# Performance work log

Measured on AMD Instinct MI355X. Metric: run time of the kernel, lower is better.

Reference implementation:

```python
import jax, jax.numpy as jnp
import numpy as np
from jax import lax

LBDA = 0.1
EPS = 0.01
NUM_CLASSES = 20


def setup_inputs() -> dict:
    key = jax.random.key(0)
    k1, k2 = jax.random.split(key)
    target_features = jax.random.normal(k1, (2048, 8, 2048), dtype=jnp.float32)
    support_features = jax.random.normal(k2, (100, 8, 2048), dtype=jnp.float32)
    # 20-way 5-shot: every class present so per-class mean is well defined
    support_labels = jnp.repeat(jnp.arange(NUM_CLASSES, dtype=jnp.int32), 100 // NUM_CLASSES)
    return {
        "target_features": target_features,
        "support_features": support_features,
        "support_labels": support_labels,
    }


def _softmin(xs, lbda):
    # -lbda * log(sum_i exp(-x_i/lbda)), stable
    return -lbda * jax.nn.logsumexp(jnp.stack([-x / lbda for x in xs], axis=0), axis=0)


def otam_cum_dist(dists, lbda=LBDA):
    # dists: [Q, Sp, L, S] frame distance matrices
    d = jnp.pad(dists, ((0, 0), (0, 0), (0, 0), (1, 1)))  # pad columns -> M = S + 2
    M = d.shape[-1]
    # row 0: running sum along columns (cum[0,0] = d[0,0] = 0 from padding)
    row0 = jnp.cumsum(d[:, :, 0, :], axis=-1)

    def step(prev_row, d_row):
        # prev_row, d_row: [Q, Sp, M]; column 0 is never written -> stays 0
        cur = [jnp.zeros_like(d_row[..., 0])]
        cur.append(d_row[..., 1] + _softmin([prev_row[..., 0], prev_row[..., 1], cur[0]], lbda))
        for m in range(2, M - 1):
            cur.append(d_row[..., m] + _softmin([prev_row[..., m - 1], cur[m - 1]], lbda))
        cur.append(d_row[..., M - 1] + _softmin([prev_row[..., M - 2], prev_row[..., M - 1], cur[M - 2]], lbda))
        new_row = jnp.stack(cur, axis=-1)
        return new_row, None

    d_rows = jnp.moveaxis(d[:, :, 1:, :], 2, 0)  # [L-1, Q, Sp, M]
    final_row, _ = lax.scan(step, row0, d_rows)
    return final_row[..., -1]  # [Q, Sp]


def cos_sim(x, y, eps=EPS):
    num = x @ y.T
    den = jnp.linalg.norm(x, axis=-1)[:, None] * jnp.linalg.norm(y, axis=-1)[None, :] + eps
    return num / den


def reference(target_features, support_features, support_labels):
    Q, S, D = target_features.shape
    Sp = support_features.shape[0]
    tf = target_features.reshape(Q * S, D)
    sf = support_features.reshape(Sp * S, D)
    frame_dists = 1.0 - cos_sim(tf, sf)  # [Q*S, Sp*S]
    # '(tb ts) (sb ss) -> tb sb ts ss'
    dists = frame_dists.reshape(Q, S, Sp, S).transpose(0, 2, 1, 3)
    cum_dists = otam_cum_dist(dists) + otam_cum_dist(dists.transpose(0, 1, 3, 2))  # [Q, Sp]
    # per-class mean over support (torch.unique returns sorted labels 0..C-1)
    onehot = (support_labels[:, None] == jnp.arange(NUM_CLASSES)[None, :]).astype(cum_dists.dtype)
    onehot = onehot / jnp.sum(onehot, axis=0, keepdims=True)
    class_dists = cum_dists @ onehot  # [Q, C]
    return -class_dists[None]  # logits [1, Q, C]
```

## Files before the change

### kernel.cpp

```cpp
#include <hip/hip_runtime.h>

#define QN    2048
#define SS    8
#define DD    2048
#define SP    100
#define NCLS  20
#define MROWS (QN*SS)
#define NROWS (SP*SS)
#define NPAD  896
#define KK    DD

typedef __bf16 bf16x8 __attribute__((ext_vector_type(8)));
typedef float  f32x4  __attribute__((ext_vector_type(4)));

__device__ __forceinline__ unsigned short f2bf(float f) {
    unsigned int u = __float_as_uint(f);
    u += 0x7fffu + ((u >> 16) & 1u);
    return (unsigned short)(u >> 16);
}

__global__ void cvt_kernel(const float* __restrict__ tf, const float* __restrict__ sf,
                           unsigned short* __restrict__ Abf, unsigned short* __restrict__ Bbf,
                           float* __restrict__ nA, float* __restrict__ nB)
{
    int row = blockIdx.x;
    int tid = threadIdx.x;
    const float* src = nullptr;
    unsigned short* dst;
    float* nrm; int r;
    if (row < MROWS) { src = tf + (size_t)row * DD; dst = Abf + (size_t)row * DD; nrm = nA; r = row; }
    else {
        r = row - MROWS;
        dst = Bbf + (size_t)r * DD; nrm = nB;
        if (r < NROWS) src = sf + (size_t)r * DD;
    }
    float s = 0.f;
    union { uint4 u; unsigned short h[8]; } pk;
    if (src) {
        float4 v0 = *(const float4*)(src + tid * 8);
        float4 v1 = *(const float4*)(src + tid * 8 + 4);
        s = v0.x*v0.x + v0.y*v0.y + v0.z*v0.z + v0.w*v0.w
          + v1.x*v1.x + v1.y*v1.y + v1.z*v1.z + v1.w*v1.w;
        pk.h[0]=f2bf(v0.x); pk.h[1]=f2bf(v0.y); pk.h[2]=f2bf(v0.z); pk.h[3]=f2bf(v0.w);
        pk.h[4]=f2bf(v1.x); pk.h[5]=f2bf(v1.y); pk.h[6]=f2bf(v1.z); pk.h[7]=f2bf(v1.w);
    } else {
        pk.u = make_uint4(0, 0, 0, 0);
    }
    *(uint4*)(dst + (size_t)tid * 8) = pk.u;

    for (int o = 32; o; o >>= 1) s += __shfl_down(s, o);
    __shared__ float red[4];
    if ((tid & 63) == 0) red[tid >> 6] = s;
    __syncthreads();
    if (tid == 0) nrm[r] = sqrtf(red[0] + red[1] + red[2] + red[3]);
}

__device__ __forceinline__ void gld16(const void* g, void* l) {
    __builtin_amdgcn_global_load_lds(
        (const __attribute__((address_space(1))) unsigned int*)g,
        (__attribute__((address_space(3))) unsigned int*)l, 16, 0, 0);
}

__global__ __launch_bounds__(256, 2) void gemm_kernel(
    const unsigned short* __restrict__ A,
    const unsigned short* __restrict__ B,
    const float* __restrict__ nA, const float* __restrict__ nB,
    float* __restrict__ Dout)
{
    __shared__ __align__(16) unsigned short Als[128 * 32];
    __shared__ __align__(16) unsigned short Bls[128 * 32];
    const int mt  = blockIdx.x;
    const int nt  = blockIdx.y;
    const int tid = threadIdx.x;
    const int lane = tid & 63;
    const int w    = tid >> 6;
    const int wm   = (w & 1) * 64, wn = (w >> 1) * 64;
    const int col  = lane & 15, kg = lane >> 4;

    f32x4 acc[4][4] = {};

    const int c0 = tid, c1 = tid + 256;
    const unsigned short* Ab0 = A + (size_t)mt * 128 * KK + (size_t)(c0 >> 2) * KK + (c0 & 3) * 8;
    const unsigned short* Ab1 = A + (size_t)mt * 128 * KK + (size_t)(c1 >> 2) * KK + (c1 & 3) * 8;
    const unsigned short* Bb0 = B + (size_t)nt * 128 * KK + (size_t)(c0 >> 2) * KK + (c0 & 3) * 8;
    const unsigned short* Bb1 = B + (size_t)nt * 128 * KK + (size_t)(c1 >> 2) * KK + (c1 & 3) * 8;

    for (int kk = 0; kk < KK; kk += 32) {
        __syncthreads();
        gld16(Ab0 + kk, (char*)Als + c0 * 16);
        gld16(Ab1 + kk, (char*)Als + c1 * 16);
        gld16(Bb0 + kk, (char*)Bls + c0 * 16);
        gld16(Bb1 + kk, (char*)Bls + c1 * 16);
        __syncthreads();
        bf16x8 af[4], bfr[4];
#pragma unroll
        for (int i = 0; i < 4; i++) af[i]  = *(const bf16x8*)(Als + (wm + i * 16 + col) * 32 + kg * 8);
#pragma unroll
        for (int i = 0; i < 4; i++) bfr[i] = *(const bf16x8*)(Bls + (wn + i * 16 + col) * 32 + kg * 8);
#pragma unroll
        for (int mi = 0; mi < 4; mi++)
#pragma unroll
            for (int ni = 0; ni < 4; ni++)
                acc[mi][ni] = __builtin_amdgcn_mfma_f32_16x16x32_bf16(af[mi], bfr[ni], acc[mi][ni], 0, 0, 0);
    }

    const int mbase = mt * 128 + wm;
    const int nbase = nt * 128 + wn;
#pragma unroll
    for (int ni = 0; ni < 4; ni++) {
        int n = nbase + ni * 16 + col;
        if (n < NROWS) {
            float ny = nB[n];
#pragma unroll
            for (int mi = 0; mi < 4; mi++) {
#pragma unroll
                for (int r = 0; r < 4; r++) {
                    int m = mbase + mi * 16 + kg * 4 + r;
                    float nx = nA[m];
                    Dout[(size_t)m * NROWS + n] = 1.0f - acc[mi][ni][r] / (nx * ny + 0.01f);
                }
            }
        }
    }
}

__device__ __forceinline__ float softmin2(float a, float b) {
    float mn = fminf(a, b), mx = fmaxf(a, b);
    return mn - 0.1f * __logf(1.0f + __expf((mn - mx) * 10.0f));
}
__device__ __forceinline__ float softmin3(float a, float b, float c) {
    float mn = fminf(fminf(a, b), c);
    float sum = __expf((mn - a) * 10.0f) + __expf((mn - b) * 10.0f) + __expf((mn - c) * 10.0f);
    return mn - 0.1f * __logf(sum);
}

__global__ void dp_kernel(const float* __restrict__ dist, float* __restrict__ cum)
{
    int idx = blockIdx.x * 256 + threadIdx.x;
    int q = idx / SP, sp = idx % SP;
    float t[8][8];
    const float* base = dist + (size_t)q * 8 * NROWS + sp * 8;
#pragma unroll
    for (int i = 0; i < 8; i++) {
        float4 a = *(const float4*)(base + (size_t)i * NROWS);
        float4 b = *(const float4*)(base + (size_t)i * NROWS + 4);
        t[i][0]=a.x; t[i][1]=a.y; t[i][2]=a.z; t[i][3]=a.w;
        t[i][4]=b.x; t[i][5]=b.y; t[i][6]=b.z; t[i][7]=b.w;
    }
    float res = 0.f;
#pragma unroll
    for (int dir = 0; dir < 2; dir++) {
        float prev[10], cur[10];
        prev[0] = 0.f;
#pragma unroll
        for (int m = 1; m <= 8; m++) prev[m] = prev[m - 1] + (dir ? t[m - 1][0] : t[0][m - 1]);
        prev[9] = prev[8];
#pragma unroll
        for (int l = 1; l < 8; l++) {
            cur[0] = 0.f;
            cur[1] = (dir ? t[0][l] : t[l][0]) + softmin3(prev[0], prev[1], 0.0f);
#pragma unroll
            for (int m = 2; m <= 8; m++)
                cur[m] = (dir ? t[m - 1][l] : t[l][m - 1]) + softmin2(prev[m - 1], cur[m - 1]);
            cur[9] = softmin3(prev[8], prev[9], cur[8]);
#pragma unroll
            for (int m = 0; m < 10; m++) prev[m] = cur[m];
        }
        res += prev[9];
    }
    cum[idx] = res;
}

__global__ void cls_kernel(const float* __restrict__ cum, const int* __restrict__ labels,
                           float* __restrict__ out)
{
    int idx = blockIdx.x * 256 + threadIdx.x;
    int q = idx / NCLS, c = idx % NCLS;
    float s = 0.f; int n = 0;
    const float* row = cum + (size_t)q * SP;
    for (int sp = 0; sp < SP; sp++) {
        if (labels[sp] == c) { s += row[sp]; n++; }
    }
    out[idx] = -s / (float)n;
}

extern "C" void kernel_launch(void* const* d_in, const int* in_sizes, int n_in,
                              void* d_out, int out_size, void* d_ws, size_t ws_size,
                              hipStream_t stream)
{
    const float* tf     = (const float*)d_in[0];
    const float* sf     = (const float*)d_in[1];
    const int*   labels = (const int*)d_in[2];
    float* out = (float*)d_out;

    char* ws = (char*)d_ws;
    const size_t szA    = (size_t)MROWS * KK * 2;
    const size_t szB    = (size_t)NPAD  * KK * 2;
    const size_t szNA   = (size_t)MROWS * 4;
    const size_t szNB   = (size_t)NPAD  * 4;
    const size_t szDist = (size_t)MROWS * NROWS * 4;
    unsigned short* Abf = (unsigned short*)ws;
    unsigned short* Bbf = (unsigned short*)(ws + szA);
    float* nA   = (float*)(ws + szA + szB);
    float* nB   = (float*)(ws + szA + szB + szNA);
    float* dist = (float*)(ws + szA + szB + szNA + szNB);
    float* cum  = (float*)(ws + szA + szB + szNA + szNB + szDist);

    cvt_kernel<<<MROWS + NPAD, 256, 0, stream>>>(tf, sf, Abf, Bbf, nA, nB);
    gemm_kernel<<<dim3(128, 7), 256, 0, stream>>>(Abf, Bbf, nA, nB, dist);
    dp_kernel<<<800, 256, 0, stream>>>(dist, cum);
    cls_kernel<<<160, 256, 0, stream>>>(cum, labels, out);
}
```

Before: 319.0 us.

## Fuse OTAM DP into GEMM epilogue via LDS and swizzle LDS tiles

The GEMM epilogue now writes normalized cosine distances into an LDS staging buffer. The OTAM dynamic programme runs directly from there, with lanes split by direction and the two directions combined by a shuffle. This drops the separate dp kernel and the round trip of the full fp32 distance matrix through global memory. A XOR swizzle on the k-offset of the A/B LDS tiles is also added to reduce bank conflicts. LDS per block grows to about 33KB, which may affect occupancy at two blocks per CU, and the DP now runs inside the GEMM blocks.

```diff
diff --git a/kernel.cpp b/kernel.cpp
--- a/kernel.cpp
+++ b/kernel.cpp
@@ -55,20 +55,34 @@
     if (tid == 0) nrm[r] = sqrtf(red[0] + red[1] + red[2] + red[3]);
 }
 
+__device__ __forceinline__ float softmin2(float a, float b) {
+    float mn = fminf(a, b), mx = fmaxf(a, b);
+    return mn - 0.1f * __logf(1.0f + __expf((mn - mx) * 10.0f));
+}
+__device__ __forceinline__ float softmin3(float a, float b, float c) {
+    float mn = fminf(fminf(a, b), c);
+    float sum = __expf((mn - a) * 10.0f) + __expf((mn - b) * 10.0f) + __expf((mn - c) * 10.0f);
+    return mn - 0.1f * __logf(sum);
+}
+
 __device__ __forceinline__ void gld16(const void* g, void* l) {
     __builtin_amdgcn_global_load_lds(
         (const __attribute__((address_space(1))) unsigned int*)g,
         (__attribute__((address_space(3))) unsigned int*)l, 16, 0, 0);
 }
 
+#define EPB (32 * 65)
+
 __global__ __launch_bounds__(256, 2) void gemm_kernel(
     const unsigned short* __restrict__ A,
     const unsigned short* __restrict__ B,
     const float* __restrict__ nA, const float* __restrict__ nB,
-    float* __restrict__ Dout)
-{
-    __shared__ __align__(16) unsigned short Als[128 * 32];
-    __shared__ __align__(16) unsigned short Bls[128 * 32];
+    float* __restrict__ cum)
+{
+    __shared__ __align__(16) char smem[4 * EPB * 4];
+    unsigned short* Als = (unsigned short*)smem;
+    unsigned short* Bls = Als + 128 * 32;
+
     const int mt  = blockIdx.x;
     const int nt  = blockIdx.y;
     const int tid = threadIdx.x;
@@ -80,10 +94,14 @@
     f32x4 acc[4][4] = {};
 
     const int c0 = tid, c1 = tid + 256;
-    const unsigned short* Ab0 = A + (size_t)mt * 128 * KK + (size_t)(c0 >> 2) * KK + (c0 & 3) * 8;
-    const unsigned short* Ab1 = A + (size_t)mt * 128 * KK + (size_t)(c1 >> 2) * KK + (c1 & 3) * 8;
-    const unsigned short* Bb0 = B + (size_t)nt * 128 * KK + (size_t)(c0 >> 2) * KK + (c0 & 3) * 8;
-    const unsigned short* Bb1 = B + (size_t)nt * 128 * KK + (size_t)(c1 >> 2) * KK + (c1 & 3) * 8;
+    const int r0 = c0 >> 2, k0 = ((c0 & 3) ^ ((c0 >> 3) & 3)) * 8;
+    const int r1 = c1 >> 2, k1 = ((c1 & 3) ^ ((c1 >> 3) & 3)) * 8;
+    const unsigned short* Ab0 = A + (size_t)mt * 128 * KK + (size_t)r0 * KK + k0;
+    const unsigned short* Ab1 = A + (size_t)mt * 128 * KK + (size_t)r1 * KK + k1;
+    const unsigned short* Bb0 = B + (size_t)nt * 128 * KK + (size_t)r0 * KK + k0;
+    const unsigned short* Bb1 = B + (size_t)nt * 128 * KK + (size_t)r1 * KK + k1;
+
+    const int ksw = (kg ^ ((col >> 1) & 3)) * 8;
 
     for (int kk = 0; kk < KK; kk += 32) {
         __syncthreads();
@@ -94,9 +112,9 @@
         __syncthreads();
         bf16x8 af[4], bfr[4];
 #pragma unroll
-        for (int i = 0; i < 4; i++) af[i]  = *(const bf16x8*)(Als + (wm + i * 16 + col) * 32 + kg * 8);
-#pragma unroll
-        for (int i = 0; i < 4; i++) bfr[i] = *(const bf16x8*)(Bls + (wn + i * 16 + col) * 32 + kg * 8);
+        for (int i = 0; i < 4; i++) af[i]  = *(const bf16x8*)(Als + (wm + i * 16 + col) * 32 + ksw);
+#pragma unroll
+        for (int i = 0; i < 4; i++) bfr[i] = *(const bf16x8*)(Bls + (wn + i * 16 + col) * 32 + ksw);
 #pragma unroll
         for (int mi = 0; mi < 4; mi++)
 #pragma unroll
@@ -106,69 +124,65 @@
 
     const int mbase = mt * 128 + wm;
     const int nbase = nt * 128 + wn;
-#pragma unroll
-    for (int ni = 0; ni < 4; ni++) {
-        int n = nbase + ni * 16 + col;
-        if (n < NROWS) {
-            float ny = nB[n];
-#pragma unroll
-            for (int mi = 0; mi < 4; mi++) {
-#pragma unroll
-                for (int r = 0; r < 4; r++) {
-                    int m = mbase + mi * 16 + kg * 4 + r;
-                    float nx = nA[m];
-                    Dout[(size_t)m * NROWS + n] = 1.0f - acc[mi][ni][r] / (nx * ny + 0.01f);
-                }
+    const int qv0 = mt * 16 + (wm >> 3);
+    const int sv0 = nt * 16 + (wn >> 3);
+    float* eb = (float*)smem + w * EPB;
+
+    const int qv2 = (lane >> 3) & 3;
+    const int sv  = lane & 7;
+    const int dir = lane >> 5;
+
+#pragma unroll
+    for (int p = 0; p < 2; p++) {
+        __syncthreads();
+#pragma unroll
+        for (int mi2 = 0; mi2 < 2; mi2++) {
+            const int mi = p * 2 + mi2;
+            const float nx0 = nA[mbase + mi * 16 + kg * 4 + 0];
+            const float nx1 = nA[mbase + mi * 16 + kg * 4 + 1];
+            const float nx2 = nA[mbase + mi * 16 + kg * 4 + 2];
+            const float nx3 = nA[mbase + mi * 16 + kg * 4 + 3];
+#pragma unroll
+            for (int ni = 0; ni < 4; ni++) {
+                const float ny = nB[nbase + ni * 16 + col];
+                float* dstp = eb + (mi2 * 16 + kg * 4) * 65 + ni * 16 + col;
+                dstp[0]      = 1.0f - acc[mi][ni][0] / (nx0 * ny + 0.01f);
+                dstp[65]     = 1.0f - acc[mi][ni][1] / (nx1 * ny + 0.01f);
+                dstp[130]    = 1.0f - acc[mi][ni][2] / (nx2 * ny + 0.01f);
+                dstp[195]    = 1.0f - acc[mi][ni][3] / (nx3 * ny + 0.01f);
             }
         }
-    }
-}
-
-__device__ __forceinline__ float softmin2(float a, float b) {
-    float mn = fminf(a, b), mx = fmaxf(a, b);
-    return mn - 0.1f * __logf(1.0f + __expf((mn - mx) * 10.0f));
-}
-__device__ __forceinline__ float softmin3(float a, float b, float c) {
-    float mn = fminf(fminf(a, b), c);
-    float sum = __expf((mn - a) * 10.0f) + __expf((mn - b) * 10.0f) + __expf((mn - c) * 10.0f);
-    return mn - 0.1f * __logf(sum);
-}
-
-__global__ void dp_kernel(const float* __restrict__ dist, float* __restrict__ cum)
-{
-    int idx = blockIdx.x * 256 + threadIdx.x;
-    int q = idx / SP, sp = idx % SP;
-    float t[8][8];
-    const float* base = dist + (size_t)q * 8 * NROWS + sp * 8;
-#pragma unroll
-    for (int i = 0; i < 8; i++) {
-        float4 a = *(const float4*)(base + (size_t)i * NROWS);
-        float4 b = *(const float4*)(base + (size_t)i * NROWS + 4);
-        t[i][0]=a.x; t[i][1]=a.y; t[i][2]=a.z; t[i][3]=a.w;
-        t[i][4]=b.x; t[i][5]=b.y; t[i][6]=b.z; t[i][7]=b.w;
-    }
-    float res = 0.f;
-#pragma unroll
-    for (int dir = 0; dir < 2; dir++) {
+        __syncthreads();
+
+        const float* tb = eb + (qv2 * 8) * 65 + sv * 8;
         float prev[10], cur[10];
         prev[0] = 0.f;
 #pragma unroll
-        for (int m = 1; m <= 8; m++) prev[m] = prev[m - 1] + (dir ? t[m - 1][0] : t[0][m - 1]);
+        for (int m = 1; m <= 8; m++)
+            prev[m] = prev[m - 1] + (dir ? tb[(m - 1) * 65] : tb[m - 1]);
         prev[9] = prev[8];
 #pragma unroll
         for (int l = 1; l < 8; l++) {
+            float d[8];
+#pragma unroll
+            for (int j = 0; j < 8; j++) d[j] = dir ? tb[j * 65 + l] : tb[l * 65 + j];
             cur[0] = 0.f;
-            cur[1] = (dir ? t[0][l] : t[l][0]) + softmin3(prev[0], prev[1], 0.0f);
+            cur[1] = d[0] + softmin3(prev[0], prev[1], 0.0f);
 #pragma unroll
             for (int m = 2; m <= 8; m++)
-                cur[m] = (dir ? t[m - 1][l] : t[l][m - 1]) + softmin2(prev[m - 1], cur[m - 1]);
+                cur[m] = d[m - 1] + softmin2(prev[m - 1], cur[m - 1]);
             cur[9] = softmin3(prev[8], prev[9], cur[8]);
 #pragma unroll
             for (int m = 0; m < 10; m++) prev[m] = cur[m];
         }
-        res += prev[9];
-    }
-    cum[idx] = res;
+        float res = prev[9];
+        res += __shfl_down(res, 32);
+        if (dir == 0) {
+            const int qg = qv0 + p * 4 + qv2;
+            const int sg = sv0 + sv;
+            if (sg < SP) cum[(size_t)qg * SP + sg] = res;
+        }
+    }
 }
 
 __global__ void cls_kernel(const float* __restrict__ cum, const int* __restrict__ labels,
@@ -198,16 +212,13 @@
     const size_t szB    = (size_t)NPAD  * KK * 2;
     const size_t szNA   = (size_t)MROWS * 4;
     const size_t szNB   = (size_t)NPAD  * 4;
-    const size_t szDist = (size_t)MROWS * NROWS * 4;
     unsigned short* Abf = (unsigned short*)ws;
     unsigned short* Bbf = (unsigned short*)(ws + szA);
     float* nA   = (float*)(ws + szA + szB);
     float* nB   = (float*)(ws + szA + szB + szNA);
-    float* dist = (float*)(ws + szA + szB + szNA + szNB);
-    float* cum  = (float*)(ws + szA + szB + szNA + szNB + szDist);
+    float* cum  = (float*)(ws + szA + szB + szNA + szNB);
 
     cvt_kernel<<<MROWS + NPAD, 256, 0, stream>>>(tf, sf, Abf, Bbf, nA, nB);
-    gemm_kernel<<<dim3(128, 7), 256, 0, stream>>>(Abf, Bbf, nA, nB, dist);
-    dp_kernel<<<800, 256, 0, stream>>>(dist, cum);
+    gemm_kernel<<<dim3(128, 7), 256, 0, stream>>>(Abf, Bbf, nA, nB, cum);
     cls_kernel<<<160, 256, 0, stream>>>(cum, labels, out);
 }
```

New measurement: 319.1 us. Within noise of the previous version (+0.0%).
